# Performance work log

Hardware: AMD Instinct MI355X
Metric: run time of the kernel (lower is better)

The kernel has to match this reference:

```python
import jax, jax.numpy as jnp
import numpy as np

N = 50000   # nodes
D = 128     # hidden_channels
E = 625000  # edges (before self-loops)
NEG_SLOPE = 0.2


def setup_inputs() -> dict:
    key = jax.random.key(0)
    ks = jax.random.split(key, 10)
    s = 1.0 / np.sqrt(D)
    return {
        "x": jax.random.normal(ks[0], (N, D), dtype=jnp.float32),
        "edge_index": jax.random.randint(ks[1], (2, E), 0, N, dtype=jnp.int64),
        "W1": jax.random.normal(ks[2], (D, D), dtype=jnp.float32) * s,
        "a_src1": jax.random.normal(ks[3], (D,), dtype=jnp.float32) * s,
        "a_dst1": jax.random.normal(ks[4], (D,), dtype=jnp.float32) * s,
        "b1": jax.random.normal(ks[5], (D,), dtype=jnp.float32) * 0.01,
        "W2": jax.random.normal(ks[6], (D, D), dtype=jnp.float32) * s,
        "a_src2": jax.random.normal(ks[7], (D,), dtype=jnp.float32) * s,
        "a_dst2": jax.random.normal(ks[8], (D,), dtype=jnp.float32) * s,
        "b2": jax.random.normal(ks[9], (D,), dtype=jnp.float32) * 0.01,
    }


def gat_layer(x, src, dst, W, a_src, a_dst, b):
    # x: [N, D]; src/dst: [E'] (self-loops already appended)
    h = x @ W                                   # [N, D]
    s_src = h @ a_src                           # [N]
    s_dst = h @ a_dst                           # [N]
    e = s_src[src] + s_dst[dst]                 # [E'] per-edge logits
    e = jnp.where(e > 0, e, NEG_SLOPE * e)      # leaky_relu
    # softmax over incoming edges of each dst node (self-loops -> no empty segments)
    m = jax.ops.segment_max(e, dst, num_segments=N)
    p = jnp.exp(e - m[dst])
    z = jax.ops.segment_sum(p, dst, num_segments=N)
    alpha = p / (z[dst] + 1e-16)                # [E']
    out = jax.ops.segment_sum(alpha[:, None] * h[src], dst, num_segments=N)
    return out + b


def reference(x, edge_index, W1, a_src1, a_dst1, b1, W2, a_src2, a_dst2, b2):
    loop = jnp.arange(N, dtype=edge_index.dtype)
    src = jnp.concatenate([edge_index[0], loop])
    dst = jnp.concatenate([edge_index[1], loop])
    h = jax.nn.relu(gat_layer(x, src, dst, W1, a_src1, a_dst1, b1))
    return gat_layer(h, src, dst, W2, a_src2, a_dst2, b2)
```

## Files before the change

kernel.cpp:

```cpp
#include <hip/hip_runtime.h>
#include <hip/hip_fp16.h>

#define D 128
#define NEG_SLOPE 0.2f
#define WT_STRIDE 136

typedef __attribute__((ext_vector_type(8))) _Float16 v8h;
typedef __attribute__((ext_vector_type(4))) float v4f;


__global__ __launch_bounds__(256) void partial_kernel(const int* __restrict__ deg,
                                                      int* __restrict__ psum, int N) {
  __shared__ int s[256];
  int t = threadIdx.x;
  int i = blockIdx.x * 256 + t;
  s[t] = (i < N) ? deg[i] : 0;
  __syncthreads();
  #pragma unroll
  for (int o = 128; o; o >>= 1) { if (t < o) s[t] += s[t + o]; __syncthreads(); }
  if (t == 0) psum[blockIdx.x] = s[0];
}

__global__ __launch_bounds__(1024) void scan_partials(const int* __restrict__ psum,
                                                      int* __restrict__ bbase,
                                                      int* __restrict__ off, int NB, int N) {
  __shared__ int s[1024];
  int t = threadIdx.x;
  int v = (t < NB) ? psum[t] : 0;
  s[t] = v;
  __syncthreads();
  for (int o = 1; o < 1024; o <<= 1) {
    int u = (t >= o) ? s[t - o] : 0;
    __syncthreads();
    s[t] += u;
    __syncthreads();
  }
  if (t < NB) bbase[t] = s[t] - v;
  if (t == 1023) off[N] = s[1023];
}

__global__ __launch_bounds__(256) void offs_kernel(const int* __restrict__ deg,
                                                   const int* __restrict__ bbase,
                                                   int* __restrict__ off, int N) {
  __shared__ int s[256];
  int t = threadIdx.x;
  int i = blockIdx.x * 256 + t;
  int v = (i < N) ? deg[i] : 0;
  s[t] = v;
  __syncthreads();
  #pragma unroll
  for (int o = 1; o < 256; o <<= 1) {
    int u = (t >= o) ? s[t - o] : 0;
    __syncthreads();
    s[t] += u;
    __syncthreads();
  }
  if (i < N) off[i] = bbase[blockIdx.x] + s[t] - v;
}

__global__ __launch_bounds__(256) void scatter_kernel(
    const int* __restrict__ src, const int* __restrict__ dst,
    const int* __restrict__ rank, int E, int N,
    const int* __restrict__ off, int* __restrict__ csr) {
  int i = blockIdx.x * blockDim.x + threadIdx.x;
  if (i >= E + N) return;
  int s, d;
  if (i < E) { s = src[i]; d = dst[i]; } else { s = i - E; d = s; }
  csr[off[d] + rank[i]] = s;
}


__global__ __launch_bounds__(256, 2) void gemm_hist_fused(
    const float* __restrict__ Xf, const __half* __restrict__ Xh,
    const float* __restrict__ W,
    const float* __restrict__ avs, const float* __restrict__ avd,
    __half* __restrict__ H, float* __restrict__ Ss, float* __restrict__ Sd, int N,
    const int* __restrict__ dstE, int E, int* __restrict__ deg, int* __restrict__ rank,
    int nbGemm, int nbHist)
{
  if (blockIdx.x >= nbGemm) {
    if (dstE == nullptr) return;
    int b = blockIdx.x - nbGemm;
    int EP = E + N;
    int stride = nbHist * 256;
    for (int i = b * 256 + (int)threadIdx.x; i < EP; i += stride) {
      int d = (i < E) ? dstE[i] : (i - E);
      rank[i] = atomicAdd(&deg[d], 1);
    }
    return;
  }

  __shared__ _Float16 Wt[128][WT_STRIDE];
  __shared__ _Float16 wa[2][128];

  int tid = threadIdx.x;

  #pragma unroll
  for (int it = 0; it < 16; ++it) {
    int lin = it * 256 + tid;
    int k  = lin >> 5;
    int n4 = (lin & 31) * 4;
    float4 v = *(const float4*)&W[(size_t)k * D + n4];
    Wt[n4 + 0][k] = (_Float16)v.x;
    Wt[n4 + 1][k] = (_Float16)v.y;
    Wt[n4 + 2][k] = (_Float16)v.z;
    Wt[n4 + 3][k] = (_Float16)v.w;
  }
  {
    int k = tid & 127;
    const float* vec = (tid < 128) ? avs : avd;
    float s = 0.f;
    #pragma unroll 8
    for (int n = 0; n < 128; n += 4) {
      float4 wv = *(const float4*)&W[(size_t)k * D + n];
      float4 av = *(const float4*)&vec[n];
      s += wv.x * av.x + wv.y * av.y + wv.z * av.z + wv.w * av.w;
    }
    wa[tid >> 7][k] = (_Float16)s;
  }
  __syncthreads();

  int wid = tid >> 6, lane = tid & 63;
  int quad = lane >> 4, nn = lane & 15;
  int row = blockIdx.x * 64 + wid * 16 + nn;
  int rowc = min(row, N - 1);

  v4f acc[9];
  #pragma unroll
  for (int t = 0; t < 9; ++t) acc[t] = (v4f){0.f, 0.f, 0.f, 0.f};

  #pragma unroll
  for (int ks = 0; ks < 4; ++ks) {
    int k0 = ks * 32 + quad * 8;
    v8h b;
    if (Xh) {
      b = *(const v8h*)&Xh[(size_t)rowc * D + k0];
    } else {
      float4 x0 = *(const float4*)&Xf[(size_t)rowc * D + k0];
      float4 x1 = *(const float4*)&Xf[(size_t)rowc * D + k0 + 4];
      b[0] = (_Float16)x0.x; b[1] = (_Float16)x0.y;
      b[2] = (_Float16)x0.z; b[3] = (_Float16)x0.w;
      b[4] = (_Float16)x1.x; b[5] = (_Float16)x1.y;
      b[6] = (_Float16)x1.z; b[7] = (_Float16)x1.w;
    }
    #pragma unroll
    for (int t = 0; t < 8; ++t) {
      v8h a = *(const v8h*)&Wt[t * 16 + nn][k0];
      acc[t] = __builtin_amdgcn_mfma_f32_16x16x32_f16(a, b, acc[t], 0, 0, 0);
    }
    v8h awv = *(const v8h*)&wa[nn & 1][k0];
    acc[8] = __builtin_amdgcn_mfma_f32_16x16x32_f16(awv, b, acc[8], 0, 0, 0);
  }

  if (row < N) {
    #pragma unroll
    for (int t = 0; t < 8; ++t) {
      __half2 h0 = __floats2half2_rn(acc[t].x, acc[t].y);
      __half2 h1 = __floats2half2_rn(acc[t].z, acc[t].w);
      *(__half2*)&H[(size_t)row * D + t * 16 + quad * 4]     = h0;
      *(__half2*)&H[(size_t)row * D + t * 16 + quad * 4 + 2] = h1;
    }
    if (quad == 0) { Ss[row] = acc[8].x; Sd[row] = acc[8].y; }
  }
}


__global__ __launch_bounds__(256) void agg_kernel(
    const __half* __restrict__ H, const float* __restrict__ Ssrc, const float* __restrict__ Sdst,
    const int* __restrict__ off, const int* __restrict__ csr, const float* __restrict__ bias,
    float* __restrict__ outF, __half* __restrict__ outH, int N, int do_relu)
{
  int wid = threadIdx.x >> 6, lane = threadIdx.x & 63;
  int n = blockIdx.x * 4 + wid;
  if (n >= N) return;
  int st = off[n], en = off[n + 1];
  float sd = Sdst[n];

  float m = -1e30f;
  for (int j = st + lane; j < en; j += 64) {
    int s = csr[j];
    float e = Ssrc[s] + sd;
    e = e > 0.f ? e : NEG_SLOPE * e;
    m = fmaxf(m, e);
  }
  #pragma unroll
  for (int o = 32; o; o >>= 1) m = fmaxf(m, __shfl_xor(m, o));

  float z = 0.f, ax = 0.f, ay = 0.f;
  int c = lane * 2;
  for (int base = st; base < en; base += 64) {
    int j = base + lane;
    int cnt = min(64, en - base);
    float p = 0.f; int s = 0;
    if (j < en) {
      s = csr[j];
      float e = Ssrc[s] + sd;
      e = e > 0.f ? e : NEG_SLOPE * e;
      p = __expf(e - m);
    }
    z += p;
    for (int i = 0; i < cnt; i += 8) {
      float pu[8]; __half2 hv[8];
      #pragma unroll
      for (int u = 0; u < 8; ++u) {
        int idx = i + u;
        int iu = idx < cnt ? idx : cnt - 1;
        float pb = __shfl(p, iu);
        int   sb = __shfl(s, iu);
        pu[u] = idx < cnt ? pb : 0.f;
        hv[u] = *(const __half2*)&H[(size_t)sb * D + c];
      }
      #pragma unroll
      for (int u = 0; u < 8; ++u) {
        float2 f = __half22float2(hv[u]);
        ax += pu[u] * f.x; ay += pu[u] * f.y;
      }
    }
  }
  #pragma unroll
  for (int o = 32; o; o >>= 1) z += __shfl_xor(z, o);
  float inv = 1.f / (z + 1e-16f);
  float2 bv = *(const float2*)&bias[c];
  ax = ax * inv + bv.x;
  ay = ay * inv + bv.y;
  if (do_relu) { ax = fmaxf(ax, 0.f); ay = fmaxf(ay, 0.f); }
  if (outH) {
    *(__half2*)&outH[(size_t)n * D + c] = __floats2half2_rn(ax, ay);
  } else {
    *(float2*)&outF[(size_t)n * D + c] = make_float2(ax, ay);
  }
}


extern "C" void kernel_launch(void* const* d_in, const int* in_sizes, int n_in,
                              void* d_out, int out_size, void* d_ws, size_t ws_size,
                              hipStream_t stream) {
  const float* x   = (const float*)d_in[0];
  const int*   ei  = (const int*)d_in[1];
  const float* W1  = (const float*)d_in[2];
  const float* as1 = (const float*)d_in[3];
  const float* ad1 = (const float*)d_in[4];
  const float* b1  = (const float*)d_in[5];
  const float* W2  = (const float*)d_in[6];
  const float* as2 = (const float*)d_in[7];
  const float* ad2 = (const float*)d_in[8];
  const float* b2  = (const float*)d_in[9];

  int N  = in_sizes[0] / D;
  int E  = in_sizes[1] / 2;
  int EP = E + N;
  const int* src = ei;
  const int* dst = ei + E;

  char* w = (char*)d_ws;
  auto alloc = [&](size_t bytes) -> char* {
    char* p = w; w += (bytes + 511) & ~(size_t)511; return p;
  };
  int NB = (N + 255) / 256;
  int*    deg   = (int*)alloc((size_t)N * 4);
  int*    off   = (int*)alloc(((size_t)N + 1) * 4);
  int*    csr   = (int*)alloc((size_t)EP * 4);
  int*    rank  = (int*)alloc((size_t)EP * 4);
  int*    psum  = (int*)alloc((size_t)NB * 4);
  int*    bbase = (int*)alloc((size_t)NB * 4);
  float*  ssrc  = (float*)alloc((size_t)N * 4);
  float*  sdst  = (float*)alloc((size_t)N * 4);
  __half* h     = (__half*)alloc((size_t)N * D * 2);
  __half* t1h   = (__half*)alloc((size_t)N * D * 2);

  hipMemsetAsync(deg, 0, (size_t)N * 4, stream);

  int nbGemm = (N + 63) / 64;
  int nbHist = 1024;

  gemm_hist_fused<<<nbGemm + nbHist, 256, 0, stream>>>(
      x, nullptr, W1, as1, ad1, h, ssrc, sdst, N, dst, E, deg, rank, nbGemm, nbHist);

  partial_kernel<<<NB, 256, 0, stream>>>(deg, psum, N);
  scan_partials<<<1, 1024, 0, stream>>>(psum, bbase, off, NB, N);
  offs_kernel<<<NB, 256, 0, stream>>>(deg, bbase, off, N);
  scatter_kernel<<<(EP + 255) / 256, 256, 0, stream>>>(src, dst, rank, E, N, off, csr);

  agg_kernel<<<(N + 3) / 4, 256, 0, stream>>>(h, ssrc, sdst, off, csr, b1,
                                              nullptr, t1h, N, 1);
  gemm_hist_fused<<<nbGemm, 256, 0, stream>>>(
      nullptr, t1h, W2, as2, ad2, h, ssrc, sdst, N, nullptr, 0, nullptr, nullptr, nbGemm, 0);
  agg_kernel<<<(N + 3) / 4, 256, 0, stream>>>(h, ssrc, sdst, off, csr, b2,
                                              (float*)d_out, nullptr, N, 0);
}
```

Before: 247.3 us.

## Build CSR with two-level bucket sort instead of global atomic histogram

Replaces the global per-node atomic degree histogram, rank array and three-kernel scan with a two-pass bucketed counting sort. Nodes are grouped into 128-node buckets, counted with shared-memory atomics per edge chunk, and edges are scattered into buckets before a per-bucket CSR build in shared memory. It also pre-transposes W1/W2 to fp16 once so GEMM blocks load Wt with vector copies, and interleaves edge-count blocks with GEMM blocks. The goal is to cut contended global atomics and the random scatter traffic, at the cost of more small kernels and an extra psrc/pdst pass over the edges.

```diff
diff --git a/kernel.cpp b/kernel.cpp
--- a/kernel.cpp
+++ b/kernel.cpp
@@ -4,107 +4,162 @@
 #define D 128
 #define NEG_SLOPE 0.2f
 #define WT_STRIDE 136
+#define BKT_SHIFT 7
+#define NBKP 392
 
 typedef __attribute__((ext_vector_type(8))) _Float16 v8h;
 typedef __attribute__((ext_vector_type(4))) float v4f;
 
-
-__global__ __launch_bounds__(256) void partial_kernel(const int* __restrict__ deg,
-                                                      int* __restrict__ psum, int N) {
+__global__ __launch_bounds__(128) void wtrans_kernel(
+    const float* __restrict__ W1, const float* __restrict__ W2,
+    __half* __restrict__ T1, __half* __restrict__ T2) {
+  int n = blockIdx.x, k = threadIdx.x;
+  const float* W = blockIdx.y ? W2 : W1;
+  __half* T = blockIdx.y ? T2 : T1;
+  T[n * D + k] = __float2half(W[(size_t)k * D + n]);
+}
+
+__global__ __launch_bounds__(256) void tot_kernel(const int* __restrict__ cnt_g,
+                                                  int* __restrict__ tot, int nbe) {
   __shared__ int s[256];
+  int bkt = blockIdx.x, t = threadIdx.x;
+  s[t] = (t < nbe) ? cnt_g[t * NBKP + bkt] : 0;
+  __syncthreads();
+  #pragma unroll
+  for (int o = 128; o; o >>= 1) { if (t < o) s[t] += s[t + o]; __syncthreads(); }
+  if (t == 0) tot[bkt] = s[0];
+}
+
+__global__ __launch_bounds__(512) void scanb_kernel(const int* __restrict__ tot,
+                                                    int* __restrict__ bktBase,
+                                                    int* __restrict__ off,
+                                                    int nbk, int N, int EP) {
+  __shared__ int s[512];
   int t = threadIdx.x;
-  int i = blockIdx.x * 256 + t;
-  s[t] = (i < N) ? deg[i] : 0;
-  __syncthreads();
-  #pragma unroll
-  for (int o = 128; o; o >>= 1) { if (t < o) s[t] += s[t + o]; __syncthreads(); }
-  if (t == 0) psum[blockIdx.x] = s[0];
-}
-
-__global__ __launch_bounds__(1024) void scan_partials(const int* __restrict__ psum,
-                                                      int* __restrict__ bbase,
-                                                      int* __restrict__ off, int NB, int N) {
-  __shared__ int s[1024];
-  int t = threadIdx.x;
-  int v = (t < NB) ? psum[t] : 0;
+  int v = (t < nbk) ? tot[t] : 0;
   s[t] = v;
   __syncthreads();
-  for (int o = 1; o < 1024; o <<= 1) {
+  for (int o = 1; o < 512; o <<= 1) {
     int u = (t >= o) ? s[t - o] : 0;
     __syncthreads();
     s[t] += u;
     __syncthreads();
   }
-  if (t < NB) bbase[t] = s[t] - v;
-  if (t == 1023) off[N] = s[1023];
-}
-
-__global__ __launch_bounds__(256) void offs_kernel(const int* __restrict__ deg,
-                                                   const int* __restrict__ bbase,
-                                                   int* __restrict__ off, int N) {
+  if (t < nbk) bktBase[t] = s[t] - v;
+  if (t == 0) { bktBase[nbk] = EP; off[N] = EP; }
+}
+
+__global__ __launch_bounds__(256) void base_kernel(const int* __restrict__ cnt_g,
+                                                   const int* __restrict__ bktBase,
+                                                   int* __restrict__ base_g, int nbe) {
   __shared__ int s[256];
-  int t = threadIdx.x;
-  int i = blockIdx.x * 256 + t;
-  int v = (i < N) ? deg[i] : 0;
+  int bkt = blockIdx.x, t = threadIdx.x;
+  int v = (t < nbe) ? cnt_g[t * NBKP + bkt] : 0;
   s[t] = v;
   __syncthreads();
-  #pragma unroll
   for (int o = 1; o < 256; o <<= 1) {
     int u = (t >= o) ? s[t - o] : 0;
     __syncthreads();
     s[t] += u;
     __syncthreads();
   }
-  if (i < N) off[i] = bbase[blockIdx.x] + s[t] - v;
-}
-
-__global__ __launch_bounds__(256) void scatter_kernel(
-    const int* __restrict__ src, const int* __restrict__ dst,
-    const int* __restrict__ rank, int E, int N,
-    const int* __restrict__ off, int* __restrict__ csr) {
-  int i = blockIdx.x * blockDim.x + threadIdx.x;
-  if (i >= E + N) return;
-  int s, d;
-  if (i < E) { s = src[i]; d = dst[i]; } else { s = i - E; d = s; }
-  csr[off[d] + rank[i]] = s;
-}
-
-
-__global__ __launch_bounds__(256, 2) void gemm_hist_fused(
+  if (t < nbe) base_g[t * NBKP + bkt] = bktBase[bkt] + (s[t] - v);
+}
+
+__global__ __launch_bounds__(256) void bucket_scatter(
+    const int* __restrict__ srcE, const int* __restrict__ dstE, int E, int N,
+    const int* __restrict__ base_g, int* __restrict__ psrc, int* __restrict__ pdst,
+    int nbk, int nbe) {
+  __shared__ int cur[512];
+  int eid = blockIdx.x;
+  for (int t = threadIdx.x; t < nbk; t += 256) cur[t] = base_g[eid * NBKP + t];
+  __syncthreads();
+  int EP = E + N;
+  int C = (EP + nbe - 1) / nbe;
+  int st = eid * C, en = min(EP, st + C);
+  for (int i = st + (int)threadIdx.x; i < en; i += 256) {
+    int s, d;
+    if (i < E) { s = srcE[i]; d = dstE[i]; } else { s = i - E; d = s; }
+    int pos = atomicAdd(&cur[d >> BKT_SHIFT], 1);
+    psrc[pos] = s;
+    pdst[pos] = d;
+  }
+}
+
+__global__ __launch_bounds__(256) void bucket_csr(
+    const int* __restrict__ psrc, const int* __restrict__ pdst,
+    const int* __restrict__ bktBase, int* __restrict__ off, int* __restrict__ csr, int N) {
+  __shared__ int cnt[128], cur[128], tmp[128];
+  int bkt = blockIdx.x, t = threadIdx.x;
+  int node0 = bkt << BKT_SHIFT;
+  int nn = min(128, N - node0);
+  if (t < 128) cnt[t] = 0;
+  __syncthreads();
+  int st = bktBase[bkt], en = bktBase[bkt + 1];
+  for (int e = st + t; e < en; e += 256) atomicAdd(&cnt[pdst[e] - node0], 1);
+  __syncthreads();
+  if (t < 128) tmp[t] = cnt[t];
+  __syncthreads();
+  for (int o = 1; o < 128; o <<= 1) {
+    int u = (t < 128 && t >= o) ? tmp[t - o] : 0;
+    __syncthreads();
+    if (t < 128) tmp[t] += u;
+    __syncthreads();
+  }
+  if (t < 128) {
+    int excl = tmp[t] - cnt[t];
+    cur[t] = excl;
+    if (t < nn) off[node0 + t] = st + excl;
+  }
+  __syncthreads();
+  for (int e = st + t; e < en; e += 256) {
+    int r = atomicAdd(&cur[pdst[e] - node0], 1);
+    csr[st + r] = psrc[e];
+  }
+}
+
+
+__global__ __launch_bounds__(256, 2) void gemm_ec_fused(
     const float* __restrict__ Xf, const __half* __restrict__ Xh,
-    const float* __restrict__ W,
+    const float* __restrict__ W, const __half* __restrict__ WtG,
     const float* __restrict__ avs, const float* __restrict__ avd,
     __half* __restrict__ H, float* __restrict__ Ss, float* __restrict__ Sd, int N,
-    const int* __restrict__ dstE, int E, int* __restrict__ deg, int* __restrict__ rank,
-    int nbGemm, int nbHist)
+    const int* __restrict__ dstE, int E, int* __restrict__ cnt_g,
+    int nbk, int nbGemm, int nbEdge)
 {
-  if (blockIdx.x >= nbGemm) {
-    if (dstE == nullptr) return;
-    int b = blockIdx.x - nbGemm;
-    int EP = E + N;
-    int stride = nbHist * 256;
-    for (int i = b * 256 + (int)threadIdx.x; i < EP; i += stride) {
-      int d = (i < E) ? dstE[i] : (i - E);
-      rank[i] = atomicAdd(&deg[d], 1);
-    }
-    return;
-  }
-
   __shared__ _Float16 Wt[128][WT_STRIDE];
   __shared__ _Float16 wa[2][128];
+  __shared__ int cntS[512];
 
   int tid = threadIdx.x;
-
-  #pragma unroll
-  for (int it = 0; it < 16; ++it) {
+  int gemmId;
+  if (nbEdge > 0 && (int)blockIdx.x < 2 * nbEdge) {
+    if (blockIdx.x & 1) {
+      int eid = blockIdx.x >> 1;
+      for (int t = tid; t < nbk; t += 256) cntS[t] = 0;
+      __syncthreads();
+      int EP = E + N;
+      int C = (EP + nbEdge - 1) / nbEdge;
+      int st = eid * C, en = min(EP, st + C);
+      for (int i = st + tid; i < en; i += 256) {
+        int d = (i < E) ? dstE[i] : (i - E);
+        atomicAdd(&cntS[d >> BKT_SHIFT], 1);
+      }
+      __syncthreads();
+      for (int t = tid; t < nbk; t += 256) cnt_g[eid * NBKP + t] = cntS[t];
+      return;
+    }
+    gemmId = blockIdx.x >> 1;
+  } else {
+    gemmId = (nbEdge > 0) ? ((int)blockIdx.x - nbEdge) : (int)blockIdx.x;
+  }
+
+  #pragma unroll
+  for (int it = 0; it < 8; ++it) {
     int lin = it * 256 + tid;
-    int k  = lin >> 5;
-    int n4 = (lin & 31) * 4;
-    float4 v = *(const float4*)&W[(size_t)k * D + n4];
-    Wt[n4 + 0][k] = (_Float16)v.x;
-    Wt[n4 + 1][k] = (_Float16)v.y;
-    Wt[n4 + 2][k] = (_Float16)v.z;
-    Wt[n4 + 3][k] = (_Float16)v.w;
+    int n = lin >> 4;
+    int g = lin & 15;
+    *(v8h*)&Wt[n][g * 8] = *(const v8h*)&WtG[n * D + g * 8];
   }
   {
     int k = tid & 127;
@@ -122,7 +177,7 @@
 
   int wid = tid >> 6, lane = tid & 63;
   int quad = lane >> 4, nn = lane & 15;
-  int row = blockIdx.x * 64 + wid * 16 + nn;
+  int row = gemmId * 64 + wid * 16 + nn;
   int rowc = min(row, N - 1);
 
   v4f acc[9];
@@ -163,7 +218,6 @@
     if (quad == 0) { Ss[row] = acc[8].x; Sd[row] = acc[8].y; }
   }
 }
-
 
 __global__ __launch_bounds__(256) void agg_kernel(
     const __half* __restrict__ H, const float* __restrict__ Ssrc, const float* __restrict__ Sdst,
@@ -252,39 +306,46 @@
   const int* src = ei;
   const int* dst = ei + E;
 
+  int nbk = (N + 127) >> BKT_SHIFT;
+  int nbe = 256;
+  int nbGemm = (N + 63) / 64;
+
   char* w = (char*)d_ws;
   auto alloc = [&](size_t bytes) -> char* {
     char* p = w; w += (bytes + 511) & ~(size_t)511; return p;
   };
-  int NB = (N + 255) / 256;
-  int*    deg   = (int*)alloc((size_t)N * 4);
-  int*    off   = (int*)alloc(((size_t)N + 1) * 4);
-  int*    csr   = (int*)alloc((size_t)EP * 4);
-  int*    rank  = (int*)alloc((size_t)EP * 4);
-  int*    psum  = (int*)alloc((size_t)NB * 4);
-  int*    bbase = (int*)alloc((size_t)NB * 4);
-  float*  ssrc  = (float*)alloc((size_t)N * 4);
-  float*  sdst  = (float*)alloc((size_t)N * 4);
-  __half* h     = (__half*)alloc((size_t)N * D * 2);
-  __half* t1h   = (__half*)alloc((size_t)N * D * 2);
-
-  hipMemsetAsync(deg, 0, (size_t)N * 4, stream);
-
-  int nbGemm = (N + 63) / 64;
-  int nbHist = 1024;
-
-  gemm_hist_fused<<<nbGemm + nbHist, 256, 0, stream>>>(
-      x, nullptr, W1, as1, ad1, h, ssrc, sdst, N, dst, E, deg, rank, nbGemm, nbHist);
-
-  partial_kernel<<<NB, 256, 0, stream>>>(deg, psum, N);
-  scan_partials<<<1, 1024, 0, stream>>>(psum, bbase, off, NB, N);
-  offs_kernel<<<NB, 256, 0, stream>>>(deg, bbase, off, N);
-  scatter_kernel<<<(EP + 255) / 256, 256, 0, stream>>>(src, dst, rank, E, N, off, csr);
+  __half* wtg1   = (__half*)alloc((size_t)D * D * 2);
+  __half* wtg2   = (__half*)alloc((size_t)D * D * 2);
+  int*    cnt_g  = (int*)alloc((size_t)nbe * NBKP * 4);
+  int*    base_g = (int*)alloc((size_t)nbe * NBKP * 4);
+  int*    tot    = (int*)alloc((size_t)NBKP * 4);
+  int*    bktB   = (int*)alloc((size_t)(NBKP + 1) * 4);
+  int*    off    = (int*)alloc(((size_t)N + 1) * 4);
+  int*    csr    = (int*)alloc((size_t)EP * 4);
+  int*    psrc   = (int*)alloc((size_t)EP * 4);
+  int*    pdst   = (int*)alloc((size_t)EP * 4);
+  float*  ssrc   = (float*)alloc((size_t)N * 4);
+  float*  sdst   = (float*)alloc((size_t)N * 4);
+  __half* h      = (__half*)alloc((size_t)N * D * 2);
+  __half* t1h    = (__half*)alloc((size_t)N * D * 2);
+
+  wtrans_kernel<<<dim3(D, 2), D, 0, stream>>>(W1, W2, wtg1, wtg2);
+
+  gemm_ec_fused<<<nbGemm + nbe, 256, 0, stream>>>(
+      x, nullptr, W1, wtg1, as1, ad1, h, ssrc, sdst, N,
+      dst, E, cnt_g, nbk, nbGemm, nbe);
+
+  tot_kernel<<<nbk, 256, 0, stream>>>(cnt_g, tot, nbe);
+  scanb_kernel<<<1, 512, 0, stream>>>(tot, bktB, off, nbk, N, EP);
+  base_kernel<<<nbk, 256, 0, stream>>>(cnt_g, bktB, base_g, nbe);
+  bucket_scatter<<<nbe, 256, 0, stream>>>(src, dst, E, N, base_g, psrc, pdst, nbk, nbe);
+  bucket_csr<<<nbk, 256, 0, stream>>>(psrc, pdst, bktB, off, csr, N);
 
   agg_kernel<<<(N + 3) / 4, 256, 0, stream>>>(h, ssrc, sdst, off, csr, b1,
                                               nullptr, t1h, N, 1);
-  gemm_hist_fused<<<nbGemm, 256, 0, stream>>>(
-      nullptr, t1h, W2, as2, ad2, h, ssrc, sdst, N, nullptr, 0, nullptr, nullptr, nbGemm, 0);
+  gemm_ec_fused<<<nbGemm, 256, 0, stream>>>(
+      nullptr, t1h, W2, wtg2, as2, ad2, h, ssrc, sdst, N,
+      nullptr, 0, nullptr, nbk, nbGemm, 0);
   agg_kernel<<<(N + 3) / 4, 256, 0, stream>>>(h, ssrc, sdst, off, csr, b2,
                                               (float*)d_out, nullptr, N, 0);
 }
```

Result: slower. 253.4 us (+2.5%).
